# Performance work log

Measured on AMD Instinct MI355X. Metric: run time of the kernel, lower is better.

## Reference

```python
import jax, jax.numpy as jnp
import numpy as np

EPSILON = 0.01        # temperature
DIST_THRESH = 0.2
NUM_ITERS = 8         # sparse_rebalance_iters (== num_iters here)
TOPK = 64             # topk_support
NEG_INF = -1e9


def setup_inputs() -> dict:
    key = jax.random.key(0)
    k1, k2, k3 = jax.random.split(key, 3)
    B, N, M, D = 4, 4096, 4096, 128
    return {
        "source_feats": jax.random.normal(k1, (B, N, D), dtype=jnp.float32),
        "source_locs": jax.random.uniform(k2, (B, N, 2), dtype=jnp.float32),
        "target_locs": jax.random.uniform(k3, (B, M, 2), dtype=jnp.float32),
        "source_valid_mask": jnp.ones((B, N), dtype=bool),
        "target_valid_mask": jnp.ones((B, M), dtype=bool),
    }


def _sinkhorn_attn(source_locs, target_locs, source_valid_mask, target_valid_mask):
    # pairwise squared distances: [B, M, N]
    diff = target_locs[:, :, None, :] - source_locs[:, None, :, :]
    dist_sq = jnp.sum(diff * diff, axis=-1)
    log_k = -dist_sq / (EPSILON + 1e-8)
    valid = (dist_sq < DIST_THRESH ** 2)
    valid = valid & source_valid_mask[:, None, :] & target_valid_mask[:, :, None]

    B, M, N = valid.shape
    topk = min(TOPK, N)
    if topk < N:
        masked_log_k = jnp.where(valid, log_k, NEG_INF)
        _, topk_idx = jax.lax.top_k(masked_log_k, topk)  # [B, M, topk]
        support = jnp.zeros_like(valid).at[
            jnp.arange(B)[:, None, None], jnp.arange(M)[None, :, None], topk_idx
        ].set(True)
        valid = valid & support

    log_k = jnp.where(valid, log_k, NEG_INF)

    v = jnp.zeros((B, 1, N), dtype=log_k.dtype)
    u = jnp.zeros((B, M, 1), dtype=log_k.dtype)
    for _ in range(NUM_ITERS):
        u = -jax.nn.logsumexp(log_k + v, axis=2, keepdims=True)
        v = -jax.nn.logsumexp(log_k + u, axis=1, keepdims=True)
        v = jnp.where(source_valid_mask[:, None, :], v, 0.0)

    attn = jnp.exp(log_k + u + v)              # [B, M, N]
    has_source = valid.any(axis=-1, keepdims=True)  # [B, M, 1]
    return attn, has_source


def reference(source_feats, source_locs, target_locs, source_valid_mask, target_valid_mask):
    attn, has_source = _sinkhorn_attn(source_locs, target_locs,
                                      source_valid_mask, target_valid_mask)
    target_feats = jnp.einsum('bmn,bnd->bmd', attn, source_feats)
    target_feats = target_feats * target_valid_mask[:, :, None].astype(target_feats.dtype)
    target_feats = target_feats * has_source.astype(target_feats.dtype)
    return target_feats
```

## Files before the change

kernel.cpp:

```cpp
#include <hip/hip_runtime.h>
#include <math.h>

#define B 4
#define N 4096
#define M 4096
#define D 128
#define K 64
#define BT 256
#define WPB 4
#define RPW 4
#define CAP 768
#define CUTCAP 128
#define PC 128
#define EPS_DENOM 0.01000001f
#define THRESH2 0.04f
#define GC 16

__global__ __launch_bounds__(1024) void k_sort(const float* __restrict__ slocs,
        float4* __restrict__ sPack, int* __restrict__ cellStart,
        int* __restrict__ colcnt, int* __restrict__ E, int* __restrict__ R,
        float* __restrict__ extraF, float* __restrict__ cs){
    __shared__ int hist[256], startS[256], fill[256], wtot[4];
    __shared__ float2 loc[N];
    __shared__ unsigned short scell[N];
    const int b = blockIdx.x, tid = threadIdx.x;
    const int lane = tid & 63, w = tid >> 6;
    const float2* slp = (const float2*)(slocs + (size_t)b * N * 2);

    for (int i = tid; i < N; i += 1024){
        colcnt[b * N + i] = 0;
        cs[b * N + i] = 1.0f;
    }
    if (b == 0){
        if (tid < B){ E[tid] = 0; R[tid] = 0; }
        if (tid < B * D) extraF[tid] = 0.f;
    }

    if (tid < 256){ hist[tid] = 0; fill[tid] = 0; }
    __syncthreads();
    for (int i = tid; i < N; i += 1024){
        float2 p = slp[i];
        int cx = min(GC - 1, max(0, (int)(p.x * (float)GC)));
        int cy = min(GC - 1, max(0, (int)(p.y * (float)GC)));
        int cell = cy * GC + cx;
        loc[i] = p; scell[i] = (unsigned short)cell;
        atomicAdd(&hist[cell], 1);
    }
    __syncthreads();
    int hv = (tid < 256) ? hist[tid] : 0;
    int pre = hv;
    #pragma unroll
    for (int o = 1; o < 64; o <<= 1){ int t2 = __shfl_up(pre, o, 64); if (lane >= o) pre += t2; }
    if (tid < 256 && lane == 63) wtot[w] = pre;
    __syncthreads();
    if (tid < 256){
        int off = 0;
        for (int i = 0; i < w; ++i) off += wtot[i];
        int st = off + pre - hv;
        startS[tid] = st;
        cellStart[b * 257 + tid] = st;
    }
    if (tid == 0) cellStart[b * 257 + 256] = N;
    __syncthreads();
    for (int i = tid; i < N; i += 1024){
        int cell = scell[i];
        int pos = startS[cell] + atomicAdd(&fill[cell], 1);
        float2 p = loc[i];
        sPack[(size_t)b * N + pos] = make_float4(p.x, p.y, __int_as_float(i), 0.f);
    }
}

__global__ __launch_bounds__(BT, 4) void k_build(const float4* __restrict__ sPack,
        const int* __restrict__ cellStart, const float* __restrict__ tlocs,
        float* __restrict__ elkA, int* __restrict__ idxA, int* __restrict__ cnt,
        int* __restrict__ colcnt, float* __restrict__ cscElk, int* __restrict__ cscRow,
        int* __restrict__ R){
    __shared__ int cs[257];
    __shared__ float cd2[WPB][CAP];
    __shared__ int   cn [WPB][CAP];
    __shared__ int   hist[WPB][64];
    __shared__ float cutd[WPB][CUTCAP];
    __shared__ int   cutn[WPB][CUTCAP];

    const int bid  = blockIdx.x;
    const int b    = bid / (M / (WPB * RPW));
    const int m00  = (bid % (M / (WPB * RPW))) * (WPB * RPW);
    const int tid  = threadIdx.x;
    const int w    = tid >> 6;
    const int lane = tid & 63;
    const unsigned long long pmask = (lane == 0) ? 0ull : ((1ull << lane) - 1);
    const float4* sp = sPack + (size_t)b * N;

    for (int i = tid; i < 257; i += BT) cs[i] = cellStart[b * 257 + i];
    __syncthreads();

    for (int r = 0; r < RPW; ++r){
        const int m     = m00 + w * RPW + r;
        const int rowid = b * M + m;

        hist[w][lane] = 0;

        const float tx = tlocs[((size_t)b * M + m) * 2 + 0];
        const float ty = tlocs[((size_t)b * M + m) * 2 + 1];
        const int cy0 = max(0, (int)floorf((ty - 0.2f) * (float)GC - 0.001f));
        const int cy1 = min(GC - 1, (int)floorf((ty + 0.2f) * (float)GC + 0.001f));

        int c = 0;
        for (int cy = cy0; cy <= cy1; ++cy){
            float rowLo = cy * 0.0625f, rowHi = rowLo + 0.0625f;
            float dymin = fmaxf(0.f, fmaxf(rowLo - ty, ty - rowHi));
            float dxm = sqrtf(fmaxf(THRESH2 - dymin * dymin + 1e-5f, 0.f));
            int cx0 = max(0, (int)floorf((tx - dxm) * (float)GC - 0.001f));
            int cx1 = min(GC - 1, (int)floorf((tx + dxm) * (float)GC + 0.001f));
            int s = cs[cy * GC + cx0], e = cs[cy * GC + cx1 + 1];
            for (int j0 = s; j0 < e; j0 += 64){
                int j = j0 + lane;
                bool valid = j < e;
                float d2 = 1e9f; int n = 0;
                if (valid){
                    float4 q = sp[j];
                    float dx = __fsub_rn(tx, q.x);
                    float dy = __fsub_rn(ty, q.y);
                    d2 = __fadd_rn(__fmul_rn(dx, dx), __fmul_rn(dy, dy));
                    n = __float_as_int(q.z);
                }
                bool in = valid && (d2 < THRESH2);
                unsigned long long ml = __ballot(in);
                if (in){
                    int p = c + __popcll(ml & pmask);
                    if (p < CAP){ cd2[w][p] = d2; cn[w][p] = n; }
                    atomicAdd(&hist[w][min((int)(d2 * 1600.0f), 63)], 1);
                }
                c += __popcll(ml);
            }
        }
        const int ctot = min(c, CAP);

        int h = hist[w][lane];
        int pre = h;
        #pragma unroll
        for (int o = 1; o < 64; o <<= 1){
            int t2 = __shfl_up(pre, o, 64);
            if (lane >= o) pre += t2;
        }
        int cutB = 64, q = 0;
        if (c > K){
            unsigned long long ge = __ballot(pre >= K);
            int fb = __ffsll((long long)ge) - 1;
            cutB = fb;
            q = K - __shfl(pre - h, fb, 64);
        }

        int base = 0, cutc = 0;
        for (int i0 = 0; i0 < ctot; i0 += 64){
            int i = i0 + lane;
            bool valid = i < ctot;
            float d2 = 1e9f; int n = 0;
            if (valid){ d2 = cd2[w][i]; n = cn[w][i]; }
            int bk = valid ? min((int)(d2 * 1600.0f), 63) : 64;
            bool low = valid && (bk < cutB);
            unsigned long long ml = __ballot(low);
            if (low){
                int p = base + __popcll(ml & pmask);
                float e = expf(-(d2 / EPS_DENOM));
                elkA[(size_t)rowid * K + p] = e;
                idxA[(size_t)rowid * K + p] = n;
                int bn = b * N + n;
                int slot = atomicAdd(&colcnt[bn], 1);
                if (slot < PC){
                    cscElk[(size_t)bn * PC + slot] = e;
                    cscRow[(size_t)bn * PC + slot] = rowid;
                }
            }
            base += __popcll(ml);
            if (cutB < 64){
                bool eq = valid && (bk == cutB);
                unsigned long long me = __ballot(eq);
                if (eq){
                    int p = cutc + __popcll(me & pmask);
                    if (p < CUTCAP){ cutd[w][p] = d2; cutn[w][p] = n; }
                }
                cutc += __popcll(me);
            }
        }

        if (c > K){
            int cc = min(cutc, CUTCAP);
            for (int i0 = 0; i0 < CUTCAP; i0 += 64){
                int i = i0 + lane;
                bool sel = false; float d2i = 0.f; int ni = 0;
                if (i < cc){
                    d2i = cutd[w][i]; ni = cutn[w][i];
                    int rank = 0;
                    for (int j = 0; j < cc; ++j){
                        float dj = cutd[w][j]; int nj = cutn[w][j];
                        rank += (dj < d2i) || (dj == d2i && nj < ni);
                    }
                    sel = rank < q;
                }
                unsigned long long ms = __ballot(sel);
                if (sel){
                    int p = base + __popcll(ms & pmask);
                    float e = expf(-(d2i / EPS_DENOM));
                    elkA[(size_t)rowid * K + p] = e;
                    idxA[(size_t)rowid * K + p] = ni;
                    int bn = b * N + ni;
                    int slot = atomicAdd(&colcnt[bn], 1);
                    if (slot < PC){
                        cscElk[(size_t)bn * PC + slot] = e;
                        cscRow[(size_t)bn * PC + slot] = rowid;
                    }
                }
                base += __popcll(ms);
                if (i0 + 64 >= cc) break;
            }
            if (lane == 0) cnt[rowid] = K;
        } else {
            if (lane == 0){
                cnt[rowid] = c;
                if (c == 0) atomicAdd(&R[b], 1);
            }
        }
    }
}

__global__ __launch_bounds__(256) void k_prep(const int* __restrict__ colcnt,
        int* __restrict__ E, const float* __restrict__ feats, float* __restrict__ extraF){
    int t = blockIdx.x * blockDim.x + threadIdx.x;
    int lane = t & 63, b = t >> 12;
    int cc = colcnt[t];
    unsigned long long em = __ballot(cc == 0);
    if (lane == 0 && em) atomicAdd(&E[b], __popcll(em));
    if (cc == 0){
        for (int d = 0; d < D; ++d)
            atomicAdd(&extraF[b * D + d], feats[(size_t)t * D + d]);
    }
}

__global__ __launch_bounds__(256) void kA(const float* __restrict__ elkA,
        const int* __restrict__ idxA, const int* __restrict__ cnt,
        const float* __restrict__ cs, const int* __restrict__ E, float* __restrict__ eu){
    int t = blockIdx.x * blockDim.x + threadIdx.x;
    int W = t >> 6, lane = t & 63;
    for (int rr = 0; rr < 4; ++rr){
        int rid = W * 4 + rr;
        int b = rid >> 12;
        int c = cnt[rid];
        float s = 0.f;
        if (lane < c){
            int ix = (b << 12) + idxA[(size_t)rid * K + lane];
            s = elkA[(size_t)rid * K + lane] / cs[ix];
        }
        #pragma unroll
        for (int o = 32; o; o >>= 1) s += __shfl_xor(s, o, 64);
        int Eb = E[b];
        if (c == 0 && Eb == 0){
            if (lane == 0) eu[rid] = 0.f;
        } else {
            if (Eb > 0) s += (float)Eb;
            if (lane == 0) eu[rid] = 1.0f / s;
        }
    }
}

__global__ __launch_bounds__(256) void kB(const float* __restrict__ cscElk,
        const int* __restrict__ cscRow, const int* __restrict__ colcnt,
        const float* __restrict__ eu, const int* __restrict__ R, float* __restrict__ cs){
    int t = blockIdx.x * blockDim.x + threadIdx.x;
    int W = t >> 6, lane = t & 63;
    for (int rr = 0; rr < 4; ++rr){
        int cid = W * 4 + rr;
        int b = cid >> 12;
        int cc = min(colcnt[cid], PC);
        float s = 0.f;
        for (int p = lane; p < cc; p += 64)
            s += cscElk[(size_t)cid * PC + p] * eu[cscRow[(size_t)cid * PC + p]];
        #pragma unroll
        for (int o = 32; o; o >>= 1) s += __shfl_xor(s, o, 64);
        if (lane == 0)
            cs[cid] = s + (float)R[b];
    }
}

__global__ __launch_bounds__(128) void k_out(const float* __restrict__ feats,
        const float* __restrict__ elkA, const int* __restrict__ idxA,
        const int* __restrict__ cnt, const float* __restrict__ eu,
        const float* __restrict__ cs, const float* __restrict__ extraF,
        float* __restrict__ out){
    __shared__ float att[K];
    __shared__ int   sidx[K];
    int rid = blockIdx.x;
    int b = rid >> 12;
    int tid = threadIdx.x;
    int c = cnt[rid];
    if (tid < K){
        float a = 0.f; int ix = 0;
        if (tid < c){
            ix = idxA[(size_t)rid * K + tid];
            a = elkA[(size_t)rid * K + tid] * eu[rid] / cs[(b << 12) + ix];
        }
        att[tid] = a; sidx[tid] = ix;
    }
    __syncthreads();
    float acc = 0.f;
    if (c > 0){
        acc = extraF[b * D + tid];
        for (int k = 0; k < c; ++k)
            acc += att[k] * feats[((size_t)((b << 12) + sidx[k])) * D + tid];
    }
    out[(size_t)rid * D + tid] = acc;
}

extern "C" void kernel_launch(void* const* d_in, const int* in_sizes, int n_in,
                              void* d_out, int out_size, void* d_ws, size_t ws_size,
                              hipStream_t stream){
    const float* feats = (const float*)d_in[0];
    const float* slocs = (const float*)d_in[1];
    const float* tlocs = (const float*)d_in[2];
    float* out = (float*)d_out;

    char* w = (char*)d_ws;
    size_t off = 0;
    auto carve = [&](size_t bytes) -> void* {
        void* p = w + off;
        off += (bytes + 255) & ~(size_t)255;
        return p;
    };
    float* elkA    = (float*)carve((size_t)B * M * K * 4);
    int*   idxA    = (int*)  carve((size_t)B * M * K * 4);
    float* cscElk  = (float*)carve((size_t)B * N * PC * 4);
    int*   cscRow  = (int*)  carve((size_t)B * N * PC * 4);
    int*   cnt     = (int*)  carve((size_t)B * M * 4);
    int*   colcnt  = (int*)  carve((size_t)B * N * 4);
    float* eu      = (float*)carve((size_t)B * M * 4);
    float* cs      = (float*)carve((size_t)B * N * 4);
    int*   E       = (int*)  carve(B * 4);
    int*   R       = (int*)  carve(B * 4);
    float* extraF  = (float*)carve((size_t)B * D * 4);
    float4* sPack  = (float4*)carve((size_t)B * N * 16);
    int*   cellStart = (int*)carve((size_t)B * 257 * 4);

    k_sort<<<B, 1024, 0, stream>>>(slocs, sPack, cellStart, colcnt, E, R, extraF, cs);
    k_build<<<B * M / (WPB * RPW), BT, 0, stream>>>(sPack, cellStart, tlocs,
            elkA, idxA, cnt, colcnt, cscElk, cscRow, R);
    k_prep<<<(B * N) / 256, 256, 0, stream>>>(colcnt, E, feats, extraF);
    for (int it = 0; it < 8; ++it){
        kA<<<B * M / 16, 256, 0, stream>>>(elkA, idxA, cnt, cs, E, eu);
        kB<<<B * N / 16, 256, 0, stream>>>(cscElk, cscRow, colcnt, eu, R, cs);
    }
    k_out<<<B * M, D, 0, stream>>>(feats, elkA, idxA, cnt, eu, cs, extraF, out);
}
```

Measured before the change: 259.0 us.

## Pack sparse arrays as float2, fuse first row pass and prep, warp-per-row output

Packs the value and index of the CSR and CSC sparse structures into float2 so each entry takes one load. k_build now computes the first row normalizer itself, since cs starts at 1, which removes one kA launch. k_prep is folded into the first kB launch as extra blocks. The candidate scan is unrolled to two chunks per step, and k_out becomes one wavefront per row with shuffled weights and float2 feature loads. The main risk is correctness of E: the first kA pass no longer sees E, and the extra kB blocks update E and extraF concurrently with the column sums.

```diff
diff --git a/kernel.cpp b/kernel.cpp
--- a/kernel.cpp
+++ b/kernel.cpp
@@ -15,6 +15,8 @@
 #define EPS_DENOM 0.01000001f
 #define THRESH2 0.04f
 #define GC 16
+#define NBCOL (B * N / 16)
+#define NBPREP (B * N / 256)
 
 __global__ __launch_bounds__(1024) void k_sort(const float* __restrict__ slocs,
         float4* __restrict__ sPack, int* __restrict__ cellStart,
@@ -72,9 +74,9 @@
 
 __global__ __launch_bounds__(BT, 4) void k_build(const float4* __restrict__ sPack,
         const int* __restrict__ cellStart, const float* __restrict__ tlocs,
-        float* __restrict__ elkA, int* __restrict__ idxA, int* __restrict__ cnt,
-        int* __restrict__ colcnt, float* __restrict__ cscElk, int* __restrict__ cscRow,
-        int* __restrict__ R){
+        float2* __restrict__ csr, int* __restrict__ cnt,
+        int* __restrict__ colcnt, float2* __restrict__ csc,
+        int* __restrict__ R, float* __restrict__ eu){
     __shared__ int cs[257];
     __shared__ float cd2[WPB][CAP];
     __shared__ int   cn [WPB][CAP];
@@ -113,25 +115,31 @@
             int cx0 = max(0, (int)floorf((tx - dxm) * (float)GC - 0.001f));
             int cx1 = min(GC - 1, (int)floorf((tx + dxm) * (float)GC + 0.001f));
             int s = cs[cy * GC + cx0], e = cs[cy * GC + cx1 + 1];
-            for (int j0 = s; j0 < e; j0 += 64){
-                int j = j0 + lane;
-                bool valid = j < e;
-                float d2 = 1e9f; int n = 0;
-                if (valid){
-                    float4 q = sp[j];
-                    float dx = __fsub_rn(tx, q.x);
-                    float dy = __fsub_rn(ty, q.y);
-                    d2 = __fadd_rn(__fmul_rn(dx, dx), __fmul_rn(dy, dy));
-                    n = __float_as_int(q.z);
-                }
-                bool in = valid && (d2 < THRESH2);
-                unsigned long long ml = __ballot(in);
-                if (in){
-                    int p = c + __popcll(ml & pmask);
-                    if (p < CAP){ cd2[w][p] = d2; cn[w][p] = n; }
-                    atomicAdd(&hist[w][min((int)(d2 * 1600.0f), 63)], 1);
-                }
-                c += __popcll(ml);
+            for (int j0 = s; j0 < e; j0 += 128){
+                int ja = j0 + lane;
+                int jb = ja + 64;
+                float4 qa = sp[min(ja, N - 1)];
+                float4 qb = sp[min(jb, N - 1)];
+                float dxa = __fsub_rn(tx, qa.x), dya = __fsub_rn(ty, qa.y);
+                float d2a = __fadd_rn(__fmul_rn(dxa, dxa), __fmul_rn(dya, dya));
+                bool ina = (ja < e) && (d2a < THRESH2);
+                unsigned long long mla = __ballot(ina);
+                if (ina){
+                    int p = c + __popcll(mla & pmask);
+                    if (p < CAP){ cd2[w][p] = d2a; cn[w][p] = __float_as_int(qa.z); }
+                    atomicAdd(&hist[w][min((int)(d2a * 1600.0f), 63)], 1);
+                }
+                c += __popcll(mla);
+                float dxb = __fsub_rn(tx, qb.x), dyb = __fsub_rn(ty, qb.y);
+                float d2b = __fadd_rn(__fmul_rn(dxb, dxb), __fmul_rn(dyb, dyb));
+                bool inb = (jb < e) && (d2b < THRESH2);
+                unsigned long long mlb = __ballot(inb);
+                if (inb){
+                    int p = c + __popcll(mlb & pmask);
+                    if (p < CAP){ cd2[w][p] = d2b; cn[w][p] = __float_as_int(qb.z); }
+                    atomicAdd(&hist[w][min((int)(d2b * 1600.0f), 63)], 1);
+                }
+                c += __popcll(mlb);
             }
         }
         const int ctot = min(c, CAP);
@@ -151,6 +159,7 @@
             q = K - __shfl(pre - h, fb, 64);
         }
 
+        float rs = 0.f;
         int base = 0, cutc = 0;
         for (int i0 = 0; i0 < ctot; i0 += 64){
             int i = i0 + lane;
@@ -163,13 +172,14 @@
             if (low){
                 int p = base + __popcll(ml & pmask);
                 float e = expf(-(d2 / EPS_DENOM));
-                elkA[(size_t)rowid * K + p] = e;
-                idxA[(size_t)rowid * K + p] = n;
+                rs += e;
+                float2 pr; pr.x = e; pr.y = __int_as_float(n);
+                csr[(size_t)rowid * K + p] = pr;
                 int bn = b * N + n;
                 int slot = atomicAdd(&colcnt[bn], 1);
                 if (slot < PC){
-                    cscElk[(size_t)bn * PC + slot] = e;
-                    cscRow[(size_t)bn * PC + slot] = rowid;
+                    float2 pc; pc.x = e; pc.y = __int_as_float(rowid);
+                    csc[(size_t)bn * PC + slot] = pc;
                 }
             }
             base += __popcll(ml);
@@ -202,13 +212,14 @@
                 if (sel){
                     int p = base + __popcll(ms & pmask);
                     float e = expf(-(d2i / EPS_DENOM));
-                    elkA[(size_t)rowid * K + p] = e;
-                    idxA[(size_t)rowid * K + p] = ni;
+                    rs += e;
+                    float2 pr; pr.x = e; pr.y = __int_as_float(ni);
+                    csr[(size_t)rowid * K + p] = pr;
                     int bn = b * N + ni;
                     int slot = atomicAdd(&colcnt[bn], 1);
                     if (slot < PC){
-                        cscElk[(size_t)bn * PC + slot] = e;
-                        cscRow[(size_t)bn * PC + slot] = rowid;
+                        float2 pc; pc.x = e; pc.y = __int_as_float(rowid);
+                        csc[(size_t)bn * PC + slot] = pc;
                     }
                 }
                 base += __popcll(ms);
@@ -221,25 +232,16 @@
                 if (c == 0) atomicAdd(&R[b], 1);
             }
         }
-    }
-}
-
-__global__ __launch_bounds__(256) void k_prep(const int* __restrict__ colcnt,
-        int* __restrict__ E, const float* __restrict__ feats, float* __restrict__ extraF){
-    int t = blockIdx.x * blockDim.x + threadIdx.x;
-    int lane = t & 63, b = t >> 12;
-    int cc = colcnt[t];
-    unsigned long long em = __ballot(cc == 0);
-    if (lane == 0 && em) atomicAdd(&E[b], __popcll(em));
-    if (cc == 0){
-        for (int d = 0; d < D; ++d)
-            atomicAdd(&extraF[b * D + d], feats[(size_t)t * D + d]);
-    }
-}
-
-__global__ __launch_bounds__(256) void kA(const float* __restrict__ elkA,
-        const int* __restrict__ idxA, const int* __restrict__ cnt,
-        const float* __restrict__ cs, const int* __restrict__ E, float* __restrict__ eu){
+
+        #pragma unroll
+        for (int o = 32; o; o >>= 1) rs += __shfl_xor(rs, o, 64);
+        if (lane == 0) eu[rowid] = (c == 0) ? 0.f : 1.0f / rs;
+    }
+}
+
+__global__ __launch_bounds__(256) void kA(const float2* __restrict__ csr,
+        const int* __restrict__ cnt, const float* __restrict__ cs,
+        const int* __restrict__ E, float* __restrict__ eu){
     int t = blockIdx.x * blockDim.x + threadIdx.x;
     int W = t >> 6, lane = t & 63;
     for (int rr = 0; rr < 4; ++rr){
@@ -248,8 +250,8 @@
         int c = cnt[rid];
         float s = 0.f;
         if (lane < c){
-            int ix = (b << 12) + idxA[(size_t)rid * K + lane];
-            s = elkA[(size_t)rid * K + lane] / cs[ix];
+            float2 q = csr[(size_t)rid * K + lane];
+            s = q.x / cs[(b << 12) + __float_as_int(q.y)];
         }
         #pragma unroll
         for (int o = 32; o; o >>= 1) s += __shfl_xor(s, o, 64);
@@ -263,9 +265,22 @@
     }
 }
 
-__global__ __launch_bounds__(256) void kB(const float* __restrict__ cscElk,
-        const int* __restrict__ cscRow, const int* __restrict__ colcnt,
-        const float* __restrict__ eu, const int* __restrict__ R, float* __restrict__ cs){
+__global__ __launch_bounds__(256) void kB(const float2* __restrict__ csc,
+        const int* __restrict__ colcnt, const float* __restrict__ eu,
+        const int* __restrict__ R, float* __restrict__ cs,
+        const float* __restrict__ feats, float* __restrict__ extraF, int* __restrict__ E){
+    if (blockIdx.x >= NBCOL){
+        int t = (blockIdx.x - NBCOL) * 256 + threadIdx.x;
+        int lane = t & 63, b = t >> 12;
+        int cc = colcnt[t];
+        unsigned long long em = __ballot(cc == 0);
+        if (lane == 0 && em) atomicAdd(&E[b], __popcll(em));
+        if (cc == 0){
+            for (int d = 0; d < D; ++d)
+                atomicAdd(&extraF[b * D + d], feats[(size_t)t * D + d]);
+        }
+        return;
+    }
     int t = blockIdx.x * blockDim.x + threadIdx.x;
     int W = t >> 6, lane = t & 63;
     for (int rr = 0; rr < 4; ++rr){
@@ -273,8 +288,10 @@
         int b = cid >> 12;
         int cc = min(colcnt[cid], PC);
         float s = 0.f;
-        for (int p = lane; p < cc; p += 64)
-            s += cscElk[(size_t)cid * PC + p] * eu[cscRow[(size_t)cid * PC + p]];
+        for (int p = lane; p < cc; p += 64){
+            float2 q = csc[(size_t)cid * PC + p];
+            s += q.x * eu[__float_as_int(q.y)];
+        }
         #pragma unroll
         for (int o = 32; o; o >>= 1) s += __shfl_xor(s, o, 64);
         if (lane == 0)
@@ -282,33 +299,33 @@
     }
 }
 
-__global__ __launch_bounds__(128) void k_out(const float* __restrict__ feats,
-        const float* __restrict__ elkA, const int* __restrict__ idxA,
-        const int* __restrict__ cnt, const float* __restrict__ eu,
-        const float* __restrict__ cs, const float* __restrict__ extraF,
-        float* __restrict__ out){
-    __shared__ float att[K];
-    __shared__ int   sidx[K];
-    int rid = blockIdx.x;
+__global__ __launch_bounds__(256) void k_out(const float* __restrict__ feats,
+        const float2* __restrict__ csr, const int* __restrict__ cnt,
+        const float* __restrict__ eu, const float* __restrict__ cs,
+        const float* __restrict__ extraF, float* __restrict__ out){
+    int t = blockIdx.x * blockDim.x + threadIdx.x;
+    int rid = t >> 6, lane = t & 63;
     int b = rid >> 12;
-    int tid = threadIdx.x;
     int c = cnt[rid];
-    if (tid < K){
-        float a = 0.f; int ix = 0;
-        if (tid < c){
-            ix = idxA[(size_t)rid * K + tid];
-            a = elkA[(size_t)rid * K + tid] * eu[rid] / cs[(b << 12) + ix];
-        }
-        att[tid] = a; sidx[tid] = ix;
-    }
-    __syncthreads();
-    float acc = 0.f;
-    if (c > 0){
-        acc = extraF[b * D + tid];
-        for (int k = 0; k < c; ++k)
-            acc += att[k] * feats[((size_t)((b << 12) + sidx[k])) * D + tid];
-    }
-    out[(size_t)rid * D + tid] = acc;
+    float a = 0.f; int ix = (b << 12);
+    if (lane < c){
+        float2 q = csr[(size_t)rid * K + lane];
+        ix = (b << 12) + __float_as_int(q.y);
+        a = q.x * eu[rid] / cs[ix];
+    }
+    float2 acc = make_float2(0.f, 0.f);
+    if (c > 0)
+        acc = ((const float2*)extraF)[b * 64 + lane];
+    const float2* fb = (const float2*)feats;
+    #pragma unroll 4
+    for (int k = 0; k < c; ++k){
+        float ak = __shfl(a, k, 64);
+        int  nk = __shfl(ix, k, 64);
+        float2 f = fb[(size_t)nk * 64 + lane];
+        acc.x = fmaf(ak, f.x, acc.x);
+        acc.y = fmaf(ak, f.y, acc.y);
+    }
+    ((float2*)out)[(size_t)rid * 64 + lane] = acc;
 }
 
 extern "C" void kernel_launch(void* const* d_in, const int* in_sizes, int n_in,
@@ -326,10 +343,8 @@
         off += (bytes + 255) & ~(size_t)255;
         return p;
     };
-    float* elkA    = (float*)carve((size_t)B * M * K * 4);
-    int*   idxA    = (int*)  carve((size_t)B * M * K * 4);
-    float* cscElk  = (float*)carve((size_t)B * N * PC * 4);
-    int*   cscRow  = (int*)  carve((size_t)B * N * PC * 4);
+    float2* csr    = (float2*)carve((size_t)B * M * K * 8);
+    float2* csc    = (float2*)carve((size_t)B * N * PC * 8);
     int*   cnt     = (int*)  carve((size_t)B * M * 4);
     int*   colcnt  = (int*)  carve((size_t)B * N * 4);
     float* eu      = (float*)carve((size_t)B * M * 4);
@@ -342,11 +357,11 @@
 
     k_sort<<<B, 1024, 0, stream>>>(slocs, sPack, cellStart, colcnt, E, R, extraF, cs);
     k_build<<<B * M / (WPB * RPW), BT, 0, stream>>>(sPack, cellStart, tlocs,
-            elkA, idxA, cnt, colcnt, cscElk, cscRow, R);
-    k_prep<<<(B * N) / 256, 256, 0, stream>>>(colcnt, E, feats, extraF);
-    for (int it = 0; it < 8; ++it){
-        kA<<<B * M / 16, 256, 0, stream>>>(elkA, idxA, cnt, cs, E, eu);
-        kB<<<B * N / 16, 256, 0, stream>>>(cscElk, cscRow, colcnt, eu, R, cs);
-    }
-    k_out<<<B * M, D, 0, stream>>>(feats, elkA, idxA, cnt, eu, cs, extraF, out);
-}
+            csr, cnt, colcnt, csc, R, eu);
+    kB<<<NBCOL + NBPREP, 256, 0, stream>>>(csc, colcnt, eu, R, cs, feats, extraF, E);
+    for (int it = 2; it <= 8; ++it){
+        kA<<<B * M / 16, 256, 0, stream>>>(csr, cnt, cs, E, eu);
+        kB<<<NBCOL, 256, 0, stream>>>(csc, colcnt, eu, R, cs, feats, extraF, E);
+    }
+    k_out<<<B * M / 4, 256, 0, stream>>>(feats, csr, cnt, eu, cs, extraF, out);
+}
```

Result: slower. 269.5 us (+4.0%).
